# Optimization experiments

Hardware: AMD Instinct MI355X
Metric: run time of the kernel (lower is better)

Reference implementation:

```python
import jax, jax.numpy as jnp
import numpy as np

DIM_IN, DIM_K, DIM_V = 128, 64, 128

def setup_inputs() -> dict:
    key = jax.random.key(0)
    k1, k2, k3, k4 = jax.random.split(key, 4)
    x = jax.random.normal(k1, (8, DIM_IN, 4096), dtype=jnp.float32)
    # nn.Linear(dim_in, dim_out) weight has shape [dim_out, dim_in]; y @ W.T
    Wq = jax.random.normal(k2, (DIM_K, DIM_IN), dtype=jnp.float32) / np.sqrt(DIM_IN)
    Wk = jax.random.normal(k3, (DIM_K, DIM_IN), dtype=jnp.float32) / np.sqrt(DIM_IN)
    Wv = jax.random.normal(k4, (DIM_V, DIM_IN), dtype=jnp.float32) / np.sqrt(DIM_IN)
    return {"x": x, "Wq": Wq, "Wk": Wk, "Wv": Wv}

def reference(x, Wq, Wk, Wv):
    # x: [b, dim_in, n] -> y: [b, n, dim_in]
    y = jnp.swapaxes(x, -1, -2)
    q = jnp.einsum('bnd,kd->bnk', y, Wq)  # [b, n, dim_k]
    k = jnp.einsum('bnd,kd->bnk', y, Wk)  # [b, n, dim_k]
    v = jnp.einsum('bnd,vd->bnv', y, Wv)  # [b, n, dim_v]
    scale = 1.0 / np.sqrt(DIM_K).astype(np.float32)
    dist = jnp.einsum('bik,bjk->bij', q, k) * scale  # [b, n, n]
    dist = jax.nn.softmax(dist, axis=-1)
    att = jnp.einsum('bij,bjv->biv', dist, v)  # [b, n, dim_v]
    att = jnp.swapaxes(att, -1, -2)  # [b, dim_v, n]
    return att + x
```

## Files before the change

kernel.cpp:

```cpp
#include <hip/hip_runtime.h>
#include <hip/hip_bf16.h>
#include <stdint.h>

#define NB   8
#define NSEQ 4096
#define DIN  128
#define DK   64
#define DVV  128

typedef __bf16 bf16x8 __attribute__((ext_vector_type(8)));
typedef float f32x4 __attribute__((ext_vector_type(4)));
typedef float f32x2 __attribute__((ext_vector_type(2)));
typedef unsigned int u32x4v __attribute__((ext_vector_type(4)));
typedef unsigned short u16;
typedef unsigned int u32;

__device__ __forceinline__ u32 cvt_pk_bf16(float lo, float hi) {
  u32 r;
  asm("v_cvt_pk_bf16_f32 %0, %1, %2" : "=v"(r) : "v"(lo), "v"(hi));
  return r;
}

#define GLDS16(G, L)                                                          \
  __builtin_amdgcn_global_load_lds(                                           \
      (__attribute__((address_space(1))) void*)(G),                           \
      (__attribute__((address_space(3))) void*)(L), 16, 0, 0)

__global__ __launch_bounds__(256) void proj(
    const float* __restrict__ x, const float* __restrict__ Wq,
    const float* __restrict__ Wk, const float* __restrict__ Wv,
    u16* __restrict__ Qb, u16* __restrict__ Kf, u16* __restrict__ Vf) {
  __shared__ alignas(16) u16 xs[64 * 128];
  const int tid = threadIdx.x;
  const int w = tid >> 6, l = tid & 63;
  const int lg = l >> 4, li = l & 15;
  const int b = blockIdx.x & 7;
  const int n0 = (blockIdx.x >> 3) << 6;

  {
    const float* xp = x + ((size_t)b * DIN + w * 32) * NSEQ + n0 + l;
    #pragma unroll
    for (int cc = 0; cc < 4; ++cc) {
      const int c = w * 4 + cc;
      u32 pk[4];
      #pragma unroll
      for (int jj = 0; jj < 4; ++jj) {
        const float f0 = xp[(size_t)(cc * 8 + 2 * jj) * NSEQ];
        const float f1 = xp[(size_t)(cc * 8 + 2 * jj + 1) * NSEQ];
        pk[jj] = cvt_pk_bf16(f0, f1);
      }
      *(uint4*)&xs[l * 128 + ((c ^ (l & 15)) * 8)] = *(uint4*)pk;
    }
  }

  const float* W;
  float scale = 1.0f;
  if (w == 0)      { W = Wq; scale = 0.180336880111120429f; }
  else if (w == 1) { W = Wk; }
  else if (w == 2) { W = Wv; }
  else             { W = Wv + 64 * DIN; }

  bf16x8 wf[4][4];
  #pragma unroll
  for (int ct = 0; ct < 4; ++ct) {
    const float* wr = W + (ct * 16 + li) * DIN + lg * 8;
    #pragma unroll
    for (int ks = 0; ks < 4; ++ks) {
      const float4 f0 = *(const float4*)(wr + 32 * ks);
      const float4 f1 = *(const float4*)(wr + 32 * ks + 4);
      u32x4v pk;
      pk[0] = cvt_pk_bf16(f0.x * scale, f0.y * scale);
      pk[1] = cvt_pk_bf16(f0.z * scale, f0.w * scale);
      pk[2] = cvt_pk_bf16(f1.x * scale, f1.y * scale);
      pk[3] = cvt_pk_bf16(f1.z * scale, f1.w * scale);
      wf[ct][ks] = __builtin_bit_cast(bf16x8, pk);
    }
  }

  __syncthreads();

  const f32x4 fz = {0.f, 0.f, 0.f, 0.f};
  #pragma unroll
  for (int nt = 0; nt < 4; ++nt) {
    const int n16 = n0 + nt * 16;
    bf16x8 xf[4];
    #pragma unroll
    for (int ks = 0; ks < 4; ++ks)
      xf[ks] = *(const bf16x8*)&xs[(nt * 16 + li) * 128 + (((lg + 4 * ks) ^ li) * 8)];
    #pragma unroll
    for (int ct = 0; ct < 4; ++ct) {
      f32x4 acc = fz;
      if (w < 2) {
        #pragma unroll
        for (int ks = 0; ks < 4; ++ks)
          acc = __builtin_amdgcn_mfma_f32_16x16x32_bf16(xf[ks], wf[ct][ks], acc, 0, 0, 0);
        if (w == 0) {
          u16* ob = Qb + (size_t)b * NSEQ * DK;
          #pragma unroll
          for (int r = 0; r < 4; ++r)
            ob[(size_t)(n16 + lg * 4 + r) * DK + ct * 16 + li] =
                (u16)cvt_pk_bf16(acc[r], acc[r]);
        } else {
          #pragma unroll
          for (int r = 0; r < 4; ++r) {
            const int n = n16 + lg * 4 + r;
            const int t = n >> 5, rowin = n & 31;
            const int jt = (rowin >> 2) & 1;
            const int lip = 4 * (rowin >> 3) + (rowin & 3);
            const int kc = ct >> 1;
            const int lgp = ((ct & 1) * 16 + li) >> 3;
            Kf[((size_t)(b * 128 + t)) * 2048 + (jt * 2 + kc) * 512 +
               (lgp * 16 + lip) * 8 + (li & 7)] = (u16)cvt_pk_bf16(acc[r], acc[r]);
          }
        }
      } else {
        #pragma unroll
        for (int ks = 0; ks < 4; ++ks)
          acc = __builtin_amdgcn_mfma_f32_16x16x32_bf16(wf[ct][ks], xf[ks], acc, 0, 0, 0);
        const int chb = (w == 3 ? 64 : 0) + ct * 16 + lg * 4;
        #pragma unroll
        for (int r = 0; r < 4; ++r) {
          const int dv = chb + r;
          const int n = n16 + li;
          const int t = n >> 5, kv = n & 31;
          const int s = dv >> 4;
          const int lp = (dv & 7) | ((kv >> 3) << 3) | (((dv >> 3) & 1) << 5);
          Vf[((size_t)(b * 128 + t)) * 4096 + s * 512 + lp * 8 + (kv & 7)] =
              (u16)cvt_pk_bf16(acc[r], acc[r]);
        }
      }
    }
  }
}

__global__ __launch_bounds__(256, 2) void attn(
    const u16* __restrict__ Qb, const u16* __restrict__ Kf,
    const u16* __restrict__ Vf, const float* __restrict__ x,
    float* __restrict__ out) {
  __shared__ alignas(16) char lds[69632];
  const int tid = threadIdx.x;
  const int w = tid >> 6, l = tid & 63;
  const int lg = l >> 4, li = l & 15;
  const int b = blockIdx.x & 7;
  const int qbase = (blockIdx.x >> 3) << 6;

  bf16x8 qf[4][2];
  #pragma unroll
  for (int h = 0; h < 4; ++h) {
    const u16* qp = Qb + ((size_t)(b * NSEQ + qbase + h * 16 + li) * DK + lg * 8);
    qf[h][0] = *(const bf16x8*)qp;
    qf[h][1] = *(const bf16x8*)(qp + 32);
  }

  const f32x4 fzero = {0.f, 0.f, 0.f, 0.f};
  const f32x2 fz2 = {0.f, 0.f};
  f32x4 oacc[4][8];
  #pragma unroll
  for (int h = 0; h < 4; ++h)
    #pragma unroll
    for (int dt = 0; dt < 8; ++dt) oacc[h][dt] = fzero;
  f32x2 lrow2[4] = {fz2, fz2, fz2, fz2};

  const u16* kbase = Kf + (size_t)b * 128 * 2048 + l * 8;
  const u16* vbase = Vf + (size_t)b * 128 * 4096 + l * 8;
  char* const mybuf = lds + w * 16384;
  const int vq = (((li & 7) | (lg << 3) | ((li >> 3) << 5)) << 4);

  bf16x8 kf[2][2];
#define KLOAD(T) do {                                                         \
    const u16* kp_ = kbase + (size_t)(T) * 2048;                              \
    _Pragma("unroll") for (int jt = 0; jt < 2; ++jt)                          \
      _Pragma("unroll") for (int kc = 0; kc < 2; ++kc)                        \
        kf[jt][kc] = *(const bf16x8*)(kp_ + (jt * 2 + kc) * 512);             \
  } while (0)
#define STAGEV(T, B) do {                                                     \
    char* vb_ = mybuf + (B) * 8192;                                           \
    const u16* vp_ = vbase + (size_t)(T) * 4096;                              \
    _Pragma("unroll") for (int s = 0; s < 8; ++s)                             \
      GLDS16(vp_ + s * 512, vb_ + s * 1024);                                  \
  } while (0)
#define BODY(T, CUR, PREFETCH) do {                                           \
    if (PREFETCH) STAGEV((T) + 1, (CUR) ^ 1);                                 \
    bf16x8 pf[4];                                                             \
    __builtin_amdgcn_s_setprio(1);                                            \
    f32x4 sa[4], sb[4];                                                       \
    _Pragma("unroll") for (int h = 0; h < 4; ++h) {                           \
      sa[h] = __builtin_amdgcn_mfma_f32_16x16x32_bf16(kf[0][0], qf[h][0], fzero, 0, 0, 0); \
      sa[h] = __builtin_amdgcn_mfma_f32_16x16x32_bf16(kf[0][1], qf[h][1], sa[h], 0, 0, 0); \
      sb[h] = __builtin_amdgcn_mfma_f32_16x16x32_bf16(kf[1][0], qf[h][0], fzero, 0, 0, 0); \
      sb[h] = __builtin_amdgcn_mfma_f32_16x16x32_bf16(kf[1][1], qf[h][1], sb[h], 0, 0, 0); \
    }                                                                         \
    __builtin_amdgcn_s_setprio(0);                                            \
    if (PREFETCH) KLOAD((T) + 1);                                             \
    _Pragma("unroll") for (int h = 0; h < 4; ++h) {                           \
      const float p0 = __builtin_amdgcn_exp2f(sa[h][0]);                      \
      const float p1 = __builtin_amdgcn_exp2f(sa[h][1]);                      \
      const float p2 = __builtin_amdgcn_exp2f(sa[h][2]);                      \
      const float p3 = __builtin_amdgcn_exp2f(sa[h][3]);                      \
      const float p4 = __builtin_amdgcn_exp2f(sb[h][0]);                      \
      const float p5 = __builtin_amdgcn_exp2f(sb[h][1]);                      \
      const float p6 = __builtin_amdgcn_exp2f(sb[h][2]);                      \
      const float p7 = __builtin_amdgcn_exp2f(sb[h][3]);                      \
      f32x2 e0 = {p0, p1}, e1 = {p2, p3}, e2 = {p4, p5}, e3 = {p6, p7};       \
      lrow2[h] += (e0 + e1) + (e2 + e3);                    \
      u32x4v pk;                                                              \
      pk[0] = cvt_pk_bf16(p0, p1);                                            \
      pk[1] = cvt_pk_bf16(p2, p3);                                            \
      pk[2] = cvt_pk_bf16(p4, p5);                                            \
      pk[3] = cvt_pk_bf16(p6, p7);                                            \
      pf[h] = __builtin_bit_cast(bf16x8, pk);                                 \
    }                                                                         \
    asm volatile("s_waitcnt vmcnt(12)" ::: "memory");                         \
    const char* vb = mybuf + (CUR) * 8192;                                    \
    __builtin_amdgcn_s_setprio(1);                                            \
    _Pragma("unroll") for (int dt = 0; dt < 8; ++dt) {                        \
      const bf16x8 vf = *(const bf16x8*)(vb + dt * 1024 + vq);                \
      _Pragma("unroll") for (int h = 0; h < 4; ++h)                           \
        oacc[h][dt] = __builtin_amdgcn_mfma_f32_16x16x32_bf16(vf, pf[h], oacc[h][dt], 0, 0, 0); \
    }                                                                         \
    __builtin_amdgcn_s_setprio(0);                                            \
  } while (0)

  const int t0 = w * 32;
  STAGEV(t0, 0);
  KLOAD(t0);

  #pragma unroll 2
  for (int i = 0; i < 31; ++i) {
    BODY(t0 + i, i & 1, 1);
  }
  BODY(t0 + 31, 1, 0);

  float lrow[4];
  #pragma unroll
  for (int h = 0; h < 4; ++h) {
    float ls = lrow2[h].x + lrow2[h].y;
    ls += __shfl_xor(ls, 16, 64);
    ls += __shfl_xor(ls, 32, 64);
    lrow[h] = ls;
  }
  float* const bufA = (float*)lds;
  float* const bufB = (float*)(lds + 34304);
  float* const stats = (float*)(lds + 68608);
#define DUMP(DST) do {                                                        \
    _Pragma("unroll") for (int h = 0; h < 4; ++h)                             \
      _Pragma("unroll") for (int dt = 0; dt < 8; ++dt)                        \
        _Pragma("unroll") for (int r = 0; r < 4; ++r)                         \
          (DST)[(dt * 16 + lg * 4 + r) * 67 + h * 16 + li] = oacc[h][dt][r];  \
  } while (0)
#define ADDF(SRC) do {                                                        \
    _Pragma("unroll") for (int h = 0; h < 4; ++h)                             \
      _Pragma("unroll") for (int dt = 0; dt < 8; ++dt)                        \
        _Pragma("unroll") for (int r = 0; r < 4; ++r)                         \
          oacc[h][dt][r] += (SRC)[(dt * 16 + lg * 4 + r) * 67 + h * 16 + li]; \
  } while (0)
#define SAVESTATS(WI) do {                                                    \
    if (lg == 0) {                                                            \
      for (int h = 0; h < 4; ++h) stats[(WI) * 64 + h * 16 + li] = lrow[h];   \
    }                                                                         \
  } while (0)
  __syncthreads();
  if (w == 1) { DUMP(bufA); SAVESTATS(1); }
  if (w == 3) { DUMP(bufB); SAVESTATS(3); }
  __syncthreads();
  if (w == 0) ADDF(bufA);
  if (w == 2) {
    ADDF(bufB);
    #pragma unroll
    for (int h = 0; h < 4; ++h) lrow[h] += stats[3 * 64 + h * 16 + li];
  }
  __syncthreads();
  if (w == 2) { DUMP(bufA); SAVESTATS(2); }
  __syncthreads();
  if (w == 0) {
    ADDF(bufA);
    #pragma unroll
    for (int h = 0; h < 4; ++h) {
      const float ls = lrow[h] + stats[1 * 64 + h * 16 + li] + stats[2 * 64 + h * 16 + li];
      const float rl = 1.0f / ls;
      #pragma unroll
      for (int dt = 0; dt < 8; ++dt) {
        #pragma unroll
        for (int r = 0; r < 4; ++r) {
          const int dv = dt * 16 + lg * 4 + r;
          const size_t idx = ((size_t)b * DVV + dv) * NSEQ + qbase + h * 16 + li;
          out[idx] = oacc[h][dt][r] * rl + x[idx];
        }
      }
    }
  }
#undef KLOAD
#undef STAGEV
#undef BODY
#undef DUMP
#undef ADDF
#undef SAVESTATS
}

extern "C" void kernel_launch(void* const* d_in, const int* in_sizes, int n_in,
                              void* d_out, int out_size, void* d_ws, size_t ws_size,
                              hipStream_t stream) {
  const float* x  = (const float*)d_in[0];
  const float* Wq = (const float*)d_in[1];
  const float* Wk = (const float*)d_in[2];
  const float* Wv = (const float*)d_in[3];
  float* out = (float*)d_out;

  u16* qws = (u16*)d_ws;
  u16* kws = qws + (size_t)NB * NSEQ * DK;
  u16* vws = kws + (size_t)NB * NSEQ * DK;

  proj<<<512, 256, 0, stream>>>(x, Wq, Wk, Wv, qws, kws, vws);
  attn<<<512, 256, 0, stream>>>(qws, kws, vws, x, out);
}
```

Baseline: 75.96 us.

## Switch attention MFMAs from 16x16x32 to 32x32x16 with matching K/V layouts

Replaces the 16x16x32 bf16 MFMA tiles in the QK^T and PV stages with 32x32x16 tiles, and rewrites the K and V fragment layouts produced by the projection kernel to match the new operand shapes. Larger MFMA tiles reuse each operand across more outputs, so fewer instructions and fewer LDS reads are needed per unit of work, and the row-sum reduction needs fewer cross-lane shuffles. In exchange, accumulator register usage grows and the final LDS reduction and output indexing are remapped, which could affect occupancy and the store access pattern.

```diff
diff --git a/kernel.cpp b/kernel.cpp
--- a/kernel.cpp
+++ b/kernel.cpp
@@ -10,7 +10,7 @@
 
 typedef __bf16 bf16x8 __attribute__((ext_vector_type(8)));
 typedef float f32x4 __attribute__((ext_vector_type(4)));
-typedef float f32x2 __attribute__((ext_vector_type(2)));
+typedef float f32x16 __attribute__((ext_vector_type(16)));
 typedef unsigned int u32x4v __attribute__((ext_vector_type(4)));
 typedef unsigned short u16;
 typedef unsigned int u32;
@@ -104,13 +104,13 @@
           #pragma unroll
           for (int r = 0; r < 4; ++r) {
             const int n = n16 + lg * 4 + r;
-            const int t = n >> 5, rowin = n & 31;
-            const int jt = (rowin >> 2) & 1;
-            const int lip = 4 * (rowin >> 3) + (rowin & 3);
-            const int kc = ct >> 1;
-            const int lgp = ((ct & 1) * 16 + li) >> 3;
-            Kf[((size_t)(b * 128 + t)) * 2048 + (jt * 2 + kc) * 512 +
-               (lgp * 16 + lip) * 8 + (li & 7)] = (u16)cvt_pk_bf16(acc[r], acc[r]);
+            const int d = ct * 16 + li;
+            const int t = n >> 5, v = n & 31;
+            const int s = v >> 4, c = (v >> 3) & 1, j = v & 7;
+            const int m = (j & 3) + 16 * s + 8 * (j >> 2) + 4 * c;
+            const int hi = (d >> 3) & 1, ks = d >> 4, je = d & 7;
+            Kf[((size_t)(b * 128 + t) * 4 + ks) * 512 + ((hi << 5) + m) * 8 + je] =
+                (u16)cvt_pk_bf16(acc[r], acc[r]);
           }
         }
       } else {
@@ -123,9 +123,9 @@
           const int dv = chb + r;
           const int n = n16 + li;
           const int t = n >> 5, kv = n & 31;
-          const int s = dv >> 4;
-          const int lp = (dv & 7) | ((kv >> 3) << 3) | (((dv >> 3) & 1) << 5);
-          Vf[((size_t)(b * 128 + t)) * 4096 + s * 512 + lp * 8 + (kv & 7)] =
+          const int s = kv >> 4, c = (kv >> 3) & 1, j = kv & 7;
+          const int dt = dv >> 5, row = dv & 31;
+          Vf[((size_t)(b * 128 + t) * 8 + dt * 2 + s) * 512 + (c * 32 + row) * 8 + j] =
               (u16)cvt_pk_bf16(acc[r], acc[r]);
         }
       }
@@ -140,83 +140,88 @@
   __shared__ alignas(16) char lds[69632];
   const int tid = threadIdx.x;
   const int w = tid >> 6, l = tid & 63;
-  const int lg = l >> 4, li = l & 15;
+  const int lo5 = l & 31, hi5 = l >> 5;
   const int b = blockIdx.x & 7;
   const int qbase = (blockIdx.x >> 3) << 6;
 
-  bf16x8 qf[4][2];
-  #pragma unroll
-  for (int h = 0; h < 4; ++h) {
-    const u16* qp = Qb + ((size_t)(b * NSEQ + qbase + h * 16 + li) * DK + lg * 8);
-    qf[h][0] = *(const bf16x8*)qp;
-    qf[h][1] = *(const bf16x8*)(qp + 32);
-  }
-
-  const f32x4 fzero = {0.f, 0.f, 0.f, 0.f};
-  const f32x2 fz2 = {0.f, 0.f};
-  f32x4 oacc[4][8];
-  #pragma unroll
-  for (int h = 0; h < 4; ++h)
-    #pragma unroll
-    for (int dt = 0; dt < 8; ++dt) oacc[h][dt] = fzero;
-  f32x2 lrow2[4] = {fz2, fz2, fz2, fz2};
+  bf16x8 qf[2][4];
+  #pragma unroll
+  for (int qt = 0; qt < 2; ++qt) {
+    const u16* qp = Qb + ((size_t)(b * NSEQ + qbase + qt * 32 + lo5)) * DK + hi5 * 8;
+    #pragma unroll
+    for (int ks = 0; ks < 4; ++ks)
+      qf[qt][ks] = *(const bf16x8*)(qp + ks * 16);
+  }
+
+  f32x16 oacc[4][2];
+  #pragma unroll
+  for (int dt = 0; dt < 4; ++dt)
+    #pragma unroll
+    for (int qt = 0; qt < 2; ++qt)
+      #pragma unroll
+      for (int r = 0; r < 16; ++r) oacc[dt][qt][r] = 0.f;
+  const f32x16 z16 = oacc[0][0];
+  float lrow[2] = {0.f, 0.f};
 
   const u16* kbase = Kf + (size_t)b * 128 * 2048 + l * 8;
   const u16* vbase = Vf + (size_t)b * 128 * 4096 + l * 8;
   char* const mybuf = lds + w * 16384;
-  const int vq = (((li & 7) | (lg << 3) | ((li >> 3) << 5)) << 4);
-
-  bf16x8 kf[2][2];
+
+  bf16x8 kf[4];
 #define KLOAD(T) do {                                                         \
     const u16* kp_ = kbase + (size_t)(T) * 2048;                              \
-    _Pragma("unroll") for (int jt = 0; jt < 2; ++jt)                          \
-      _Pragma("unroll") for (int kc = 0; kc < 2; ++kc)                        \
-        kf[jt][kc] = *(const bf16x8*)(kp_ + (jt * 2 + kc) * 512);             \
+    _Pragma("unroll") for (int ks = 0; ks < 4; ++ks)                          \
+      kf[ks] = *(const bf16x8*)(kp_ + ks * 512);                              \
   } while (0)
 #define STAGEV(T, B) do {                                                     \
     char* vb_ = mybuf + (B) * 8192;                                           \
     const u16* vp_ = vbase + (size_t)(T) * 4096;                              \
-    _Pragma("unroll") for (int s = 0; s < 8; ++s)                             \
-      GLDS16(vp_ + s * 512, vb_ + s * 1024);                                  \
+    _Pragma("unroll") for (int f = 0; f < 8; ++f)                             \
+      GLDS16(vp_ + f * 512, vb_ + f * 1024);                                  \
   } while (0)
 #define BODY(T, CUR, PREFETCH) do {                                           \
     if (PREFETCH) STAGEV((T) + 1, (CUR) ^ 1);                                 \
-    bf16x8 pf[4];                                                             \
+    f32x16 s32[2];                                                            \
     __builtin_amdgcn_s_setprio(1);                                            \
-    f32x4 sa[4], sb[4];                                                       \
-    _Pragma("unroll") for (int h = 0; h < 4; ++h) {                           \
-      sa[h] = __builtin_amdgcn_mfma_f32_16x16x32_bf16(kf[0][0], qf[h][0], fzero, 0, 0, 0); \
-      sa[h] = __builtin_amdgcn_mfma_f32_16x16x32_bf16(kf[0][1], qf[h][1], sa[h], 0, 0, 0); \
-      sb[h] = __builtin_amdgcn_mfma_f32_16x16x32_bf16(kf[1][0], qf[h][0], fzero, 0, 0, 0); \
-      sb[h] = __builtin_amdgcn_mfma_f32_16x16x32_bf16(kf[1][1], qf[h][1], sb[h], 0, 0, 0); \
+    _Pragma("unroll") for (int qt = 0; qt < 2; ++qt) {                        \
+      s32[qt] = __builtin_amdgcn_mfma_f32_32x32x16_bf16(kf[0], qf[qt][0], z16, 0, 0, 0); \
+      s32[qt] = __builtin_amdgcn_mfma_f32_32x32x16_bf16(kf[1], qf[qt][1], s32[qt], 0, 0, 0); \
+      s32[qt] = __builtin_amdgcn_mfma_f32_32x32x16_bf16(kf[2], qf[qt][2], s32[qt], 0, 0, 0); \
+      s32[qt] = __builtin_amdgcn_mfma_f32_32x32x16_bf16(kf[3], qf[qt][3], s32[qt], 0, 0, 0); \
     }                                                                         \
     __builtin_amdgcn_s_setprio(0);                                            \
     if (PREFETCH) KLOAD((T) + 1);                                             \
-    _Pragma("unroll") for (int h = 0; h < 4; ++h) {                           \
-      const float p0 = __builtin_amdgcn_exp2f(sa[h][0]);                      \
-      const float p1 = __builtin_amdgcn_exp2f(sa[h][1]);                      \
-      const float p2 = __builtin_amdgcn_exp2f(sa[h][2]);                      \
-      const float p3 = __builtin_amdgcn_exp2f(sa[h][3]);                      \
-      const float p4 = __builtin_amdgcn_exp2f(sb[h][0]);                      \
-      const float p5 = __builtin_amdgcn_exp2f(sb[h][1]);                      \
-      const float p6 = __builtin_amdgcn_exp2f(sb[h][2]);                      \
-      const float p7 = __builtin_amdgcn_exp2f(sb[h][3]);                      \
-      f32x2 e0 = {p0, p1}, e1 = {p2, p3}, e2 = {p4, p5}, e3 = {p6, p7};       \
-      lrow2[h] += (e0 + e1) + (e2 + e3);                    \
-      u32x4v pk;                                                              \
-      pk[0] = cvt_pk_bf16(p0, p1);                                            \
-      pk[1] = cvt_pk_bf16(p2, p3);                                            \
-      pk[2] = cvt_pk_bf16(p4, p5);                                            \
-      pk[3] = cvt_pk_bf16(p6, p7);                                            \
-      pf[h] = __builtin_bit_cast(bf16x8, pk);                                 \
+    bf16x8 pf[2][2];                                                          \
+    _Pragma("unroll") for (int qt = 0; qt < 2; ++qt) {                        \
+      float pa[16];                                                           \
+      _Pragma("unroll") for (int r = 0; r < 16; ++r)                          \
+        pa[r] = __builtin_amdgcn_exp2f(s32[qt][r]);                           \
+      lrow[qt] += (((pa[0] + pa[1]) + (pa[2] + pa[3])) +                      \
+                   ((pa[4] + pa[5]) + (pa[6] + pa[7]))) +                     \
+                  (((pa[8] + pa[9]) + (pa[10] + pa[11])) +                    \
+                   ((pa[12] + pa[13]) + (pa[14] + pa[15])));                  \
+      u32x4v pk0, pk1;                                                        \
+      pk0[0] = cvt_pk_bf16(pa[0], pa[1]);                                     \
+      pk0[1] = cvt_pk_bf16(pa[2], pa[3]);                                     \
+      pk0[2] = cvt_pk_bf16(pa[4], pa[5]);                                     \
+      pk0[3] = cvt_pk_bf16(pa[6], pa[7]);                                     \
+      pk1[0] = cvt_pk_bf16(pa[8], pa[9]);                                     \
+      pk1[1] = cvt_pk_bf16(pa[10], pa[11]);                                   \
+      pk1[2] = cvt_pk_bf16(pa[12], pa[13]);                                   \
+      pk1[3] = cvt_pk_bf16(pa[14], pa[15]);                                   \
+      pf[qt][0] = __builtin_bit_cast(bf16x8, pk0);                            \
+      pf[qt][1] = __builtin_bit_cast(bf16x8, pk1);                            \
     }                                                                         \
     asm volatile("s_waitcnt vmcnt(12)" ::: "memory");                         \
     const char* vb = mybuf + (CUR) * 8192;                                    \
     __builtin_amdgcn_s_setprio(1);                                            \
-    _Pragma("unroll") for (int dt = 0; dt < 8; ++dt) {                        \
-      const bf16x8 vf = *(const bf16x8*)(vb + dt * 1024 + vq);                \
-      _Pragma("unroll") for (int h = 0; h < 4; ++h)                           \
-        oacc[h][dt] = __builtin_amdgcn_mfma_f32_16x16x32_bf16(vf, pf[h], oacc[h][dt], 0, 0, 0); \
+    _Pragma("unroll") for (int dt = 0; dt < 4; ++dt) {                        \
+      _Pragma("unroll") for (int s = 0; s < 2; ++s) {                         \
+        const bf16x8 vf = *(const bf16x8*)(vb + (dt * 2 + s) * 1024 + l * 16);\
+        _Pragma("unroll") for (int qt = 0; qt < 2; ++qt)                      \
+          oacc[dt][qt] = __builtin_amdgcn_mfma_f32_32x32x16_bf16(             \
+              vf, pf[qt][s], oacc[dt][qt], 0, 0, 0);                          \
+      }                                                                       \
     }                                                                         \
     __builtin_amdgcn_s_setprio(0);                                            \
   } while (0)
@@ -231,32 +236,30 @@
   }
   BODY(t0 + 31, 1, 0);
 
-  float lrow[4];
-  #pragma unroll
-  for (int h = 0; h < 4; ++h) {
-    float ls = lrow2[h].x + lrow2[h].y;
-    ls += __shfl_xor(ls, 16, 64);
-    ls += __shfl_xor(ls, 32, 64);
-    lrow[h] = ls;
-  }
+  #pragma unroll
+  for (int qt = 0; qt < 2; ++qt)
+    lrow[qt] += __shfl_xor(lrow[qt], 32, 64);
   float* const bufA = (float*)lds;
   float* const bufB = (float*)(lds + 34304);
   float* const stats = (float*)(lds + 68608);
 #define DUMP(DST) do {                                                        \
-    _Pragma("unroll") for (int h = 0; h < 4; ++h)                             \
-      _Pragma("unroll") for (int dt = 0; dt < 8; ++dt)                        \
-        _Pragma("unroll") for (int r = 0; r < 4; ++r)                         \
-          (DST)[(dt * 16 + lg * 4 + r) * 67 + h * 16 + li] = oacc[h][dt][r];  \
+    _Pragma("unroll") for (int dt = 0; dt < 4; ++dt)                          \
+      _Pragma("unroll") for (int qt = 0; qt < 2; ++qt)                        \
+        _Pragma("unroll") for (int r = 0; r < 16; ++r)                        \
+          (DST)[(dt * 32 + (r & 3) + 8 * (r >> 2) + 4 * hi5) * 67 +           \
+                qt * 32 + lo5] = oacc[dt][qt][r];                             \
   } while (0)
 #define ADDF(SRC) do {                                                        \
-    _Pragma("unroll") for (int h = 0; h < 4; ++h)                             \
-      _Pragma("unroll") for (int dt = 0; dt < 8; ++dt)                        \
-        _Pragma("unroll") for (int r = 0; r < 4; ++r)                         \
-          oacc[h][dt][r] += (SRC)[(dt * 16 + lg * 4 + r) * 67 + h * 16 + li]; \
+    _Pragma("unroll") for (int dt = 0; dt < 4; ++dt)                          \
+      _Pragma("unroll") for (int qt = 0; qt < 2; ++qt)                        \
+        _Pragma("unroll") for (int r = 0; r < 16; ++r)                        \
+          oacc[dt][qt][r] += (SRC)[(dt * 32 + (r & 3) + 8 * (r >> 2) + 4 * hi5) * 67 + \
+                                   qt * 32 + lo5];                            \
   } while (0)
 #define SAVESTATS(WI) do {                                                    \
-    if (lg == 0) {                                                            \
-      for (int h = 0; h < 4; ++h) stats[(WI) * 64 + h * 16 + li] = lrow[h];   \
+    if (l < 32) {                                                             \
+      for (int qt = 0; qt < 2; ++qt)                                          \
+        stats[(WI) * 64 + qt * 32 + lo5] = lrow[qt];                          \
     }                                                                         \
   } while (0)
   __syncthreads();
@@ -267,7 +270,7 @@
   if (w == 2) {
     ADDF(bufB);
     #pragma unroll
-    for (int h = 0; h < 4; ++h) lrow[h] += stats[3 * 64 + h * 16 + li];
+    for (int qt = 0; qt < 2; ++qt) lrow[qt] += stats[3 * 64 + qt * 32 + lo5];
   }
   __syncthreads();
   if (w == 2) { DUMP(bufA); SAVESTATS(2); }
@@ -275,16 +278,17 @@
   if (w == 0) {
     ADDF(bufA);
     #pragma unroll
-    for (int h = 0; h < 4; ++h) {
-      const float ls = lrow[h] + stats[1 * 64 + h * 16 + li] + stats[2 * 64 + h * 16 + li];
+    for (int qt = 0; qt < 2; ++qt) {
+      const float ls = lrow[qt] + stats[1 * 64 + qt * 32 + lo5]
+                                + stats[2 * 64 + qt * 32 + lo5];
       const float rl = 1.0f / ls;
       #pragma unroll
-      for (int dt = 0; dt < 8; ++dt) {
+      for (int dt = 0; dt < 4; ++dt) {
         #pragma unroll
-        for (int r = 0; r < 4; ++r) {
-          const int dv = dt * 16 + lg * 4 + r;
-          const size_t idx = ((size_t)b * DVV + dv) * NSEQ + qbase + h * 16 + li;
-          out[idx] = oacc[h][dt][r] * rl + x[idx];
+        for (int r = 0; r < 16; ++r) {
+          const int dv = dt * 32 + (r & 3) + 8 * (r >> 2) + 4 * hi5;
+          const size_t idx = ((size_t)b * DVV + dv) * NSEQ + qbase + qt * 32 + lo5;
+          out[idx] = oacc[dt][qt][r] * rl + x[idx];
         }
       }
     }
```

Result: slower. 181.8 us (+139.3%).

## Split attention waves into 2 query groups x 2 KV halves with shared V staging

Applied to the files above, without the earlier changes.

Reorganizes the attention block so each pair of waves shares a 32-row query slice and splits the KV range into two halves, instead of each wave covering all 64 queries over a quarter of the keys. V tiles are staged cooperatively into LDS shared by the two query-group waves, with a barrier per iteration. This halves per-wave accumulator registers and LDS, allowing 3 blocks per CU, and simplifies the cross-wave reduction to one exchange. The cost is a block-wide barrier every iteration and doubled K loads per query group.

```diff
diff --git a/kernel.cpp b/kernel.cpp
--- a/kernel.cpp
+++ b/kernel.cpp
@@ -10,7 +10,6 @@
 
 typedef __bf16 bf16x8 __attribute__((ext_vector_type(8)));
 typedef float f32x4 __attribute__((ext_vector_type(4)));
-typedef float f32x2 __attribute__((ext_vector_type(2)));
 typedef unsigned int u32x4v __attribute__((ext_vector_type(4)));
 typedef unsigned short u16;
 typedef unsigned int u32;
@@ -104,13 +103,14 @@
           #pragma unroll
           for (int r = 0; r < 4; ++r) {
             const int n = n16 + lg * 4 + r;
+            const int d = ct * 16 + li;
             const int t = n >> 5, rowin = n & 31;
             const int jt = (rowin >> 2) & 1;
             const int lip = 4 * (rowin >> 3) + (rowin & 3);
-            const int kc = ct >> 1;
-            const int lgp = ((ct & 1) * 16 + li) >> 3;
-            Kf[((size_t)(b * 128 + t)) * 2048 + (jt * 2 + kc) * 512 +
-               (lgp * 16 + lip) * 8 + (li & 7)] = (u16)cvt_pk_bf16(acc[r], acc[r]);
+            const int kc = d >> 5;
+            const int lgp = (d & 31) >> 3;
+            Kf[((size_t)(b * 128 + t) * 4 + (jt * 2 + kc)) * 512 +
+               (lgp * 16 + lip) * 8 + (d & 7)] = (u16)cvt_pk_bf16(acc[r], acc[r]);
           }
         }
       } else {
@@ -125,7 +125,7 @@
           const int t = n >> 5, kv = n & 31;
           const int s = dv >> 4;
           const int lp = (dv & 7) | ((kv >> 3) << 3) | (((dv >> 3) & 1) << 5);
-          Vf[((size_t)(b * 128 + t)) * 4096 + s * 512 + lp * 8 + (kv & 7)] =
+          Vf[((size_t)(b * 128 + t) * 8 + s) * 512 + lp * 8 + (kv & 7)] =
               (u16)cvt_pk_bf16(acc[r], acc[r]);
         }
       }
@@ -133,37 +133,38 @@
   }
 }
 
-__global__ __launch_bounds__(256, 2) void attn(
+__global__ __launch_bounds__(256, 3) void attn(
     const u16* __restrict__ Qb, const u16* __restrict__ Kf,
     const u16* __restrict__ Vf, const float* __restrict__ x,
     float* __restrict__ out) {
-  __shared__ alignas(16) char lds[69632];
+  __shared__ alignas(16) char lds[34816];
   const int tid = threadIdx.x;
   const int w = tid >> 6, l = tid & 63;
   const int lg = l >> 4, li = l & 15;
+  const int qw = w >> 1, kvh = w & 1;
   const int b = blockIdx.x & 7;
-  const int qbase = (blockIdx.x >> 3) << 6;
-
-  bf16x8 qf[4][2];
-  #pragma unroll
-  for (int h = 0; h < 4; ++h) {
+  const int qbase = ((blockIdx.x >> 3) << 6) + qw * 32;
+
+  bf16x8 qf[2][2];
+  #pragma unroll
+  for (int h = 0; h < 2; ++h) {
     const u16* qp = Qb + ((size_t)(b * NSEQ + qbase + h * 16 + li) * DK + lg * 8);
     qf[h][0] = *(const bf16x8*)qp;
     qf[h][1] = *(const bf16x8*)(qp + 32);
   }
 
   const f32x4 fzero = {0.f, 0.f, 0.f, 0.f};
-  const f32x2 fz2 = {0.f, 0.f};
-  f32x4 oacc[4][8];
-  #pragma unroll
-  for (int h = 0; h < 4; ++h)
+  f32x4 oacc[2][8];
+  #pragma unroll
+  for (int h = 0; h < 2; ++h)
     #pragma unroll
     for (int dt = 0; dt < 8; ++dt) oacc[h][dt] = fzero;
-  f32x2 lrow2[4] = {fz2, fz2, fz2, fz2};
+  float lrow[2] = {0.f, 0.f};
 
   const u16* kbase = Kf + (size_t)b * 128 * 2048 + l * 8;
   const u16* vbase = Vf + (size_t)b * 128 * 4096 + l * 8;
-  char* const mybuf = lds + w * 16384;
+  char* const vlds = lds + kvh * 16384;
+  const int qs4 = qw * 4;
   const int vq = (((li & 7) | (lg << 3) | ((li >> 3) << 5)) << 4);
 
   bf16x8 kf[2][2];
@@ -174,17 +175,18 @@
         kf[jt][kc] = *(const bf16x8*)(kp_ + (jt * 2 + kc) * 512);             \
   } while (0)
 #define STAGEV(T, B) do {                                                     \
-    char* vb_ = mybuf + (B) * 8192;                                           \
+    char* vb_ = vlds + (B) * 8192;                                            \
     const u16* vp_ = vbase + (size_t)(T) * 4096;                              \
-    _Pragma("unroll") for (int s = 0; s < 8; ++s)                             \
-      GLDS16(vp_ + s * 512, vb_ + s * 1024);                                  \
+    _Pragma("unroll") for (int f = 0; f < 4; ++f)                             \
+      GLDS16(vp_ + (qs4 + f) * 512, vb_ + (qs4 + f) * 1024);                  \
   } while (0)
 #define BODY(T, CUR, PREFETCH) do {                                           \
+    asm volatile("s_waitcnt vmcnt(4)" ::: "memory");       \
+    __builtin_amdgcn_s_barrier();                      \
     if (PREFETCH) STAGEV((T) + 1, (CUR) ^ 1);                                 \
-    bf16x8 pf[4];                                                             \
+    f32x4 sa[2], sb[2];                                                       \
     __builtin_amdgcn_s_setprio(1);                                            \
-    f32x4 sa[4], sb[4];                                                       \
-    _Pragma("unroll") for (int h = 0; h < 4; ++h) {                           \
+    _Pragma("unroll") for (int h = 0; h < 2; ++h) {                           \
       sa[h] = __builtin_amdgcn_mfma_f32_16x16x32_bf16(kf[0][0], qf[h][0], fzero, 0, 0, 0); \
       sa[h] = __builtin_amdgcn_mfma_f32_16x16x32_bf16(kf[0][1], qf[h][1], sa[h], 0, 0, 0); \
       sb[h] = __builtin_amdgcn_mfma_f32_16x16x32_bf16(kf[1][0], qf[h][0], fzero, 0, 0, 0); \
@@ -192,7 +194,8 @@
     }                                                                         \
     __builtin_amdgcn_s_setprio(0);                                            \
     if (PREFETCH) KLOAD((T) + 1);                                             \
-    _Pragma("unroll") for (int h = 0; h < 4; ++h) {                           \
+    bf16x8 pf[2];                                                             \
+    _Pragma("unroll") for (int h = 0; h < 2; ++h) {                           \
       const float p0 = __builtin_amdgcn_exp2f(sa[h][0]);                      \
       const float p1 = __builtin_amdgcn_exp2f(sa[h][1]);                      \
       const float p2 = __builtin_amdgcn_exp2f(sa[h][2]);                      \
@@ -201,8 +204,7 @@
       const float p5 = __builtin_amdgcn_exp2f(sb[h][1]);                      \
       const float p6 = __builtin_amdgcn_exp2f(sb[h][2]);                      \
       const float p7 = __builtin_amdgcn_exp2f(sb[h][3]);                      \
-      f32x2 e0 = {p0, p1}, e1 = {p2, p3}, e2 = {p4, p5}, e3 = {p6, p7};       \
-      lrow2[h] += (e0 + e1) + (e2 + e3);                    \
+      lrow[h] += ((p0 + p1) + (p2 + p3)) + ((p4 + p5) + (p6 + p7));           \
       u32x4v pk;                                                              \
       pk[0] = cvt_pk_bf16(p0, p1);                                            \
       pk[1] = cvt_pk_bf16(p2, p3);                                            \
@@ -210,81 +212,61 @@
       pk[3] = cvt_pk_bf16(p6, p7);                                            \
       pf[h] = __builtin_bit_cast(bf16x8, pk);                                 \
     }                                                                         \
-    asm volatile("s_waitcnt vmcnt(12)" ::: "memory");                         \
-    const char* vb = mybuf + (CUR) * 8192;                                    \
+    const char* vb = vlds + (CUR) * 8192;                                     \
     __builtin_amdgcn_s_setprio(1);                                            \
     _Pragma("unroll") for (int dt = 0; dt < 8; ++dt) {                        \
       const bf16x8 vf = *(const bf16x8*)(vb + dt * 1024 + vq);                \
-      _Pragma("unroll") for (int h = 0; h < 4; ++h)                           \
+      _Pragma("unroll") for (int h = 0; h < 2; ++h)                           \
         oacc[h][dt] = __builtin_amdgcn_mfma_f32_16x16x32_bf16(vf, pf[h], oacc[h][dt], 0, 0, 0); \
     }                                                                         \
     __builtin_amdgcn_s_setprio(0);                                            \
   } while (0)
 
-  const int t0 = w * 32;
+  const int t0 = kvh * 64;
   STAGEV(t0, 0);
   KLOAD(t0);
 
-  #pragma unroll 2
-  for (int i = 0; i < 31; ++i) {
+  #pragma unroll 1
+  for (int i = 0; i < 63; ++i) {
     BODY(t0 + i, i & 1, 1);
   }
-  BODY(t0 + 31, 1, 0);
-
-  float lrow[4];
-  #pragma unroll
-  for (int h = 0; h < 4; ++h) {
-    float ls = lrow2[h].x + lrow2[h].y;
-    ls += __shfl_xor(ls, 16, 64);
-    ls += __shfl_xor(ls, 32, 64);
-    lrow[h] = ls;
-  }
-  float* const bufA = (float*)lds;
-  float* const bufB = (float*)(lds + 34304);
-  float* const stats = (float*)(lds + 68608);
-#define DUMP(DST) do {                                                        \
-    _Pragma("unroll") for (int h = 0; h < 4; ++h)                             \
-      _Pragma("unroll") for (int dt = 0; dt < 8; ++dt)                        \
-        _Pragma("unroll") for (int r = 0; r < 4; ++r)                         \
-          (DST)[(dt * 16 + lg * 4 + r) * 67 + h * 16 + li] = oacc[h][dt][r];  \
-  } while (0)
-#define ADDF(SRC) do {                                                        \
-    _Pragma("unroll") for (int h = 0; h < 4; ++h)                             \
-      _Pragma("unroll") for (int dt = 0; dt < 8; ++dt)                        \
-        _Pragma("unroll") for (int r = 0; r < 4; ++r)                         \
-          oacc[h][dt][r] += (SRC)[(dt * 16 + lg * 4 + r) * 67 + h * 16 + li]; \
-  } while (0)
-#define SAVESTATS(WI) do {                                                    \
-    if (lg == 0) {                                                            \
-      for (int h = 0; h < 4; ++h) stats[(WI) * 64 + h * 16 + li] = lrow[h];   \
-    }                                                                         \
-  } while (0)
+  BODY(t0 + 63, 1, 0);
+
+  #pragma unroll
+  for (int h = 0; h < 2; ++h) {
+    lrow[h] += __shfl_xor(lrow[h], 16, 64);
+    lrow[h] += __shfl_xor(lrow[h], 32, 64);
+  }
+  float* const mybuf = (float*)(lds + qw * 16896);
+  float* const stats = (float*)(lds + 33792);
   __syncthreads();
-  if (w == 1) { DUMP(bufA); SAVESTATS(1); }
-  if (w == 3) { DUMP(bufB); SAVESTATS(3); }
+  if (kvh == 1) {
+    if (lg == 0) {
+      #pragma unroll
+      for (int h = 0; h < 2; ++h) stats[qw * 32 + h * 16 + li] = lrow[h];
+    }
+    #pragma unroll
+    for (int h = 0; h < 2; ++h)
+      #pragma unroll
+      for (int dt = 0; dt < 8; ++dt)
+        #pragma unroll
+        for (int r = 0; r < 4; ++r)
+          mybuf[(dt * 16 + lg * 4 + r) * 33 + h * 16 + li] = oacc[h][dt][r];
+  }
   __syncthreads();
-  if (w == 0) ADDF(bufA);
-  if (w == 2) {
-    ADDF(bufB);
-    #pragma unroll
-    for (int h = 0; h < 4; ++h) lrow[h] += stats[3 * 64 + h * 16 + li];
-  }
-  __syncthreads();
-  if (w == 2) { DUMP(bufA); SAVESTATS(2); }
-  __syncthreads();
-  if (w == 0) {
-    ADDF(bufA);
-    #pragma unroll
-    for (int h = 0; h < 4; ++h) {
-      const float ls = lrow[h] + stats[1 * 64 + h * 16 + li] + stats[2 * 64 + h * 16 + li];
+  if (kvh == 0) {
+    #pragma unroll
+    for (int h = 0; h < 2; ++h) {
+      const float ls = lrow[h] + stats[qw * 32 + h * 16 + li];
       const float rl = 1.0f / ls;
       #pragma unroll
       for (int dt = 0; dt < 8; ++dt) {
         #pragma unroll
         for (int r = 0; r < 4; ++r) {
           const int dv = dt * 16 + lg * 4 + r;
+          const float oB = mybuf[dv * 33 + h * 16 + li];
           const size_t idx = ((size_t)b * DVV + dv) * NSEQ + qbase + h * 16 + li;
-          out[idx] = oacc[h][dt][r] * rl + x[idx];
+          out[idx] = (oacc[h][dt][r] + oB) * rl + x[idx];
         }
       }
     }
@@ -292,9 +274,6 @@
 #undef KLOAD
 #undef STAGEV
 #undef BODY
-#undef DUMP
-#undef ADDF
-#undef SAVESTATS
 }
 
 extern "C" void kernel_launch(void* const* d_in, const int* in_sizes, int n_in,
```

Result: slower. 90.76 us (+19.5%).
